# Kernel tuning notes

Measured on AMD Instinct MI355X. Metric: run time of the kernel, lower is better.

The kernel has to match this reference:

```python
import jax, jax.numpy as jnp
import numpy as np

B, S, D = 4, 2048, 1024
H, DH = 16, 64


def setup_inputs() -> dict:
    key = jax.random.key(0)
    ks = jax.random.split(key, 5)
    x = jax.random.normal(ks[0], (B, S, D), dtype=jnp.float32)
    # causal mask: True where attention is disallowed (j > i)
    mask = jnp.triu(jnp.ones((S, S), dtype=bool), k=1)
    mask = jnp.broadcast_to(mask, (B, S, S))
    scale = 1.0 / np.sqrt(D)
    w_q = jax.random.normal(ks[1], (D, D), dtype=jnp.float32) * scale
    w_k = jax.random.normal(ks[2], (D, D), dtype=jnp.float32) * scale
    w_v = jax.random.normal(ks[3], (D, D), dtype=jnp.float32) * scale
    w_o = jax.random.normal(ks[4], (D, D), dtype=jnp.float32) * scale
    return {"x": x, "mask": mask, "w_q": w_q, "w_k": w_k, "w_v": w_v, "w_o": w_o}


def reference(x, mask, w_q, w_k, w_v, w_o):
    # torch Linear: y = x @ W.T (bias=False)
    b, s, d = x.shape
    q = (x @ w_q.T).reshape(b, s, H, DH).transpose(0, 2, 1, 3)  # [B,H,S,DH]
    k = (x @ w_k.T).reshape(b, s, H, DH).transpose(0, 2, 1, 3)
    v = (x @ w_v.T).reshape(b, s, H, DH).transpose(0, 2, 1, 3)
    inv_sqrt_dh = jnp.asarray(1.0 / np.sqrt(DH), dtype=x.dtype)
    scores = jnp.einsum('bhqd,bhkd->bhqk', q * inv_sqrt_dh, k)  # [B,H,S,S]
    scores = jnp.where(mask[:, None, :, :], -jnp.inf, scores)
    attn = jax.nn.softmax(scores, axis=-1)  # dropout is identity in eval mode
    out = jnp.einsum('bhqk,bhkd->bhqd', attn, v)  # [B,H,S,DH]
    out = out.transpose(0, 2, 1, 3).reshape(b, s, d)
    out = out @ w_o.T
    return out, attn
```

## Files before the change

kernel.cpp:

```cpp
#include <hip/hip_runtime.h>

#define DEV __device__ __forceinline__

typedef __attribute__((ext_vector_type(8))) short short8;
typedef __attribute__((ext_vector_type(4))) float f32x4;

DEV unsigned short f2bf(float f) {
  unsigned u = __builtin_bit_cast(unsigned, f);
  u += 0x7fff + ((u >> 16) & 1);
  return (unsigned short)(u >> 16);
}

DEV void gload_lds16(const void* g, void* l) {
  __builtin_amdgcn_global_load_lds(
      (const __attribute__((address_space(1))) void*)g,
      (__attribute__((address_space(3))) void*)l, 16, 0, 0);
}

#if __has_builtin(__builtin_amdgcn_exp2f)
#define EXP2F(x) __builtin_amdgcn_exp2f(x)
#else
#define EXP2F(x) exp2f(x)
#endif

#define LOG2E 1.4426950408889634f
#define QSCALE (0.125f * LOG2E)
#define MFMA16(a, b, c) __builtin_amdgcn_mfma_f32_16x16x32_bf16((a), (b), (c), 0, 0, 0)

__global__ void cvt_f32_bf16(const float* __restrict__ in, unsigned short* __restrict__ out, int n4) {
  int i = blockIdx.x * blockDim.x + threadIdx.x;
  int stride = gridDim.x * blockDim.x;
  for (; i < n4; i += stride) {
    float4 v = ((const float4*)in)[i];
    ushort4 o;
    o.x = f2bf(v.x); o.y = f2bf(v.y); o.z = f2bf(v.z); o.w = f2bf(v.w);
    ((ushort4*)out)[i] = o;
  }
}

__global__ void cvt_w4(const float* __restrict__ w0, const float* __restrict__ w1,
                       const float* __restrict__ w2, const float* __restrict__ w3,
                       unsigned short* __restrict__ o0, unsigned short* __restrict__ o1,
                       unsigned short* __restrict__ o2, unsigned short* __restrict__ o3) {
  int i = blockIdx.x * blockDim.x + threadIdx.x;
  int sel = i >> 18, j = i & 0x3ffff;
  const float* in = sel == 0 ? w0 : sel == 1 ? w1 : sel == 2 ? w2 : w3;
  unsigned short* out = sel == 0 ? o0 : sel == 1 ? o1 : sel == 2 ? o2 : o3;
  float4 v = ((const float4*)in)[j];
  ushort4 o;
  o.x = f2bf(v.x); o.y = f2bf(v.y); o.z = f2bf(v.z); o.w = f2bf(v.w);
  ((ushort4*)out)[j] = o;
}

#define GK 1024
template <int MODE>
DEV void gemm_body(const unsigned short* A, const unsigned short* Bw, void* Cout,
                   int bx, int by) {
  __shared__ unsigned short Ash[128 * 32];
  __shared__ unsigned short Bsh[128 * 32];
  const int tid = threadIdx.x;
  const int lane = tid & 63;
  const int w = tid >> 6;
  const int wm = w >> 1, wn = w & 1;
  const int l15 = lane & 15, l4 = lane >> 4;
  const int row0 = by * 128;
  const int col0 = bx * 128;

  f32x4 acc[4][4] = {};

  for (int kt = 0; kt < GK; kt += 32) {
    __syncthreads();
#pragma unroll
    for (int c = 0; c < 2; ++c) {
      int o = c * 4096 + tid * 16;
      int ldsoff = c * 4096 + w * 1024;
      int row = o >> 6, colb = o & 63;
      gload_lds16((const char*)A + (size_t)(row0 + row) * 2048 + kt * 2 + colb,
                  (char*)Ash + ldsoff);
      gload_lds16((const char*)Bw + (size_t)(col0 + row) * 2048 + kt * 2 + colb,
                  (char*)Bsh + ldsoff);
    }
    __syncthreads();
    short8 af[4], bf[4];
#pragma unroll
    for (int m = 0; m < 4; ++m)
      af[m] = *(const short8*)((const char*)Ash + (wm * 64 + m * 16 + l15) * 64 + l4 * 16);
#pragma unroll
    for (int n = 0; n < 4; ++n)
      bf[n] = *(const short8*)((const char*)Bsh + (wn * 64 + n * 16 + l15) * 64 + l4 * 16);
#pragma unroll
    for (int m = 0; m < 4; ++m)
#pragma unroll
      for (int n = 0; n < 4; ++n)
        acc[m][n] = MFMA16(af[m], bf[n], acc[m][n]);
  }

#pragma unroll
  for (int m = 0; m < 4; ++m)
#pragma unroll
    for (int n = 0; n < 4; ++n)
#pragma unroll
      for (int r = 0; r < 4; ++r) {
        int mrow = row0 + wm * 64 + m * 16 + l4 * 4 + r;
        int ncol = col0 + wn * 64 + n * 16 + l15;
        float v = acc[m][n][r];
        if (MODE == 0) {
          ((unsigned short*)Cout)[(size_t)mrow * 1024 + ncol] = f2bf(v);
        } else if (MODE == 1) {
          int b = mrow >> 11, s = mrow & 2047, h = ncol >> 6, d = ncol & 63;
          ((unsigned short*)Cout)[((size_t)((b * 16 + h) * 64 + d)) * 2048 + s] = f2bf(v);
        } else if (MODE == 2) {
          ((float*)Cout)[(size_t)mrow * 1024 + ncol] = v;
        } else {
          ((unsigned short*)Cout)[(size_t)mrow * 1024 + ncol] = f2bf(v * QSCALE);
        }
      }
}

__global__ __launch_bounds__(256) void gemm_qkv(const unsigned short* __restrict__ A,
                                                const unsigned short* __restrict__ Wq,
                                                const unsigned short* __restrict__ Wk,
                                                const unsigned short* __restrict__ Wv,
                                                unsigned short* __restrict__ Qo,
                                                unsigned short* __restrict__ Ko,
                                                unsigned short* __restrict__ Vto) {
  const int z = blockIdx.z;
  if (z == 0)      gemm_body<3>(A, Wq, Qo,  blockIdx.x, blockIdx.y);
  else if (z == 1) gemm_body<0>(A, Wk, Ko,  blockIdx.x, blockIdx.y);
  else             gemm_body<1>(A, Wv, Vto, blockIdx.x, blockIdx.y);
}

__global__ __launch_bounds__(256) void gemm_out(const unsigned short* __restrict__ A,
                                                const unsigned short* __restrict__ Bw,
                                                float* __restrict__ Cout) {
  gemm_body<2>(A, Bw, Cout, blockIdx.x, blockIdx.y);
}


DEV void stage_tile(const unsigned short* src_base, size_t row_stride, int col0,
                    char* ldsbase, int tid) {
  const int w = tid >> 6;
  const int r0 = tid >> 3;
  const int c0 = (tid & 7) ^ (r0 & 7);
  gload_lds16((const char*)(src_base + (size_t)r0 * row_stride + col0 + c0 * 8),
              ldsbase + w * 1024);
  const int r1 = 32 + r0;
  gload_lds16((const char*)(src_base + (size_t)r1 * row_stride + col0 + c0 * 8),
              ldsbase + 4096 + w * 1024);
}

__global__ __launch_bounds__(256, 4) void attn_fused(const unsigned short* __restrict__ Q,
                                                     const unsigned short* __restrict__ Kb,
                                                     const unsigned short* __restrict__ Vt,
                                                     float* __restrict__ attn,
                                                     unsigned short* __restrict__ O) {
  __shared__ char lds[40960];

  const int tid = threadIdx.x, lane = tid & 63, w = tid >> 6;
  const int l15 = lane & 15, l4 = lane >> 4;
  const int s7 = l15 & 7;
  const int off0 = (l4 ^ s7) << 4;
  const int off1 = ((l4 + 4) ^ s7) << 4;
  const int F = blockIdx.x;
  const int xcd = F & 7, slot = F >> 3;
  const int g = slot >> 4, r = slot & 15;
  const int pr = ((g >> 1) & 1) ? (15 - r) : r;
  const int bh = xcd + (g << 3);
  const int b = bh >> 4, h = bh & 15;

  const int qt0 = pr, qt1 = 31 - pr;
  const int q00 = qt0 * 64 + w * 16, q01 = qt1 * 64 + w * 16;
  const int myq0 = q00 + l15, myq1 = q01 + l15;

  const size_t qk_base = ((size_t)b * 2048) * 1024 + h * 64;
  const unsigned short* Qp = Q + qk_base;
  const unsigned short* Kp = Kb + qk_base;
  const unsigned short* Vp = Vt + (size_t)bh * 64 * 2048;
  float* Ap = attn + (size_t)bh * 2048 * 2048;
  char* pbase = lds + 32768 + w * 2048;

  float inv_l0, inv_l1;
  {
    short8 qf0[2], qf1[2];
    {
      const char* qrow0 = (const char*)(Qp + (size_t)myq0 * 1024);
      qf0[0] = *(const short8*)(qrow0 + (l4 * 8) * 2);
      qf0[1] = *(const short8*)(qrow0 + (32 + l4 * 8) * 2);
      const char* qrow1 = (const char*)(Qp + (size_t)myq1 * 1024);
      qf1[0] = *(const short8*)(qrow1 + (l4 * 8) * 2);
      qf1[1] = *(const short8*)(qrow1 + (32 + l4 * 8) * 2);
    }
    float lacc0[4] = {0.f, 0.f, 0.f, 0.f};
    float lacc1[4] = {0.f, 0.f, 0.f, 0.f};
    stage_tile(Kp, 1024, 0, lds, tid);
    stage_tile(Kp + (size_t)64 * 1024, 1024, 0, lds + 8192, tid);
    __syncthreads();
    const int nst = (qt1 + 2) >> 1;
    for (int st = 0; st < nst; ++st) {
      char* kbb = lds + (st & 1) * 16384;
      const int jt0 = 2 * st;
      if (jt0 + 2 <= qt1) {
        char* nb = lds + ((st + 1) & 1) * 16384;
        stage_tile(Kp + (size_t)(jt0 + 2) * 64 * 1024, 1024, 0, nb, tid);
        if (jt0 + 3 <= qt1)
          stage_tile(Kp + (size_t)(jt0 + 3) * 64 * 1024, 1024, 0, nb + 8192, tid);
      }
#pragma unroll
      for (int u = 0; u < 2; ++u) {
        const int jt = jt0 + u;
        if (jt > qt1) break;
        const char* kb = kbb + u * 8192;
        const int jbase = jt * 64;
        const bool diag1 = (jt == qt1);
        const bool do0 = (jt <= qt0);
        const bool diag0 = (jt == qt0);
#pragma unroll
        for (int jb = 0; jb < 4; ++jb) {
          const char* krow = kb + (jb * 16 + l15) * 128;
          short8 k0 = *(const short8*)(krow + off0);
          short8 k1 = *(const short8*)(krow + off1);
          f32x4 a1 = {};
          a1 = MFMA16(k0, qf1[0], a1);
          a1 = MFMA16(k1, qf1[1], a1);
#pragma unroll
          for (int rr = 0; rr < 4; ++rr) {
            int j = jbase + jb * 16 + l4 * 4 + rr;
            float e = EXP2F(a1[rr]);
            lacc1[rr] += (diag1 && j > myq1) ? 0.f : e;
          }
          if (do0) {
            f32x4 a0 = {};
            a0 = MFMA16(k0, qf0[0], a0);
            a0 = MFMA16(k1, qf0[1], a0);
#pragma unroll
            for (int rr = 0; rr < 4; ++rr) {
              int j = jbase + jb * 16 + l4 * 4 + rr;
              float e = EXP2F(a0[rr]);
              lacc0[rr] += (diag0 && j > myq0) ? 0.f : e;
            }
          }
        }
      }
      __syncthreads();
    }
    float lsum0 = (lacc0[0] + lacc0[1]) + (lacc0[2] + lacc0[3]);
    lsum0 += __shfl_xor(lsum0, 16);
    lsum0 += __shfl_xor(lsum0, 32);
    float lsum1 = (lacc1[0] + lacc1[1]) + (lacc1[2] + lacc1[3]);
    lsum1 += __shfl_xor(lsum1, 16);
    lsum1 += __shfl_xor(lsum1, 32);
    inv_l0 = 1.f / lsum0;
    inv_l1 = 1.f / lsum1;
  }

  for (int t = 0; t < 2; ++t) {
    const int qt = t ? qt1 : qt0;
    const float inv_l = t ? inv_l1 : inv_l0;
    const int q0 = qt * 64 + w * 16;
    const int myq = q0 + l15;

    short8 qf[2];
    {
      const char* qrow = (const char*)(Qp + (size_t)myq * 1024);
      qf[0] = *(const short8*)(qrow + (l4 * 8) * 2);
      qf[1] = *(const short8*)(qrow + (32 + l4 * 8) * 2);
    }

    f32x4 oacc[4] = {};
    stage_tile(Kp, 1024, 0, lds, tid);
    stage_tile(Vp, 2048, 0, lds + 16384, tid);
    __syncthreads();
    for (int jt = 0; jt <= qt; ++jt) {
      const char* kb = lds + (jt & 1) * 8192;
      const char* vb = lds + 16384 + (jt & 1) * 8192;
      if (jt < qt) {
        stage_tile(Kp + (size_t)(jt + 1) * 64 * 1024, 1024, 0,
                   lds + ((jt + 1) & 1) * 8192, tid);
        stage_tile(Vp, 2048, (jt + 1) * 64, lds + 16384 + ((jt + 1) & 1) * 8192, tid);
      }
      const int jbase = jt * 64;
      const bool diag = (jt == qt);
      float p[16];
#pragma unroll
      for (int jb = 0; jb < 4; ++jb) {
        const char* krow = kb + (jb * 16 + l15) * 128;
        short8 k0 = *(const short8*)(krow + off0);
        short8 k1 = *(const short8*)(krow + off1);
        f32x4 a = {};
        a = MFMA16(k0, qf[0], a);
        a = MFMA16(k1, qf[1], a);
#pragma unroll
        for (int rr = 0; rr < 4; ++rr) {
          int j = jbase + jb * 16 + l4 * 4 + rr;
          float e = EXP2F(a[rr]) * inv_l;
          p[jb * 4 + rr] = (diag && j > myq) ? 0.f : e;
        }
      }
#pragma unroll
      for (int jb = 0; jb < 4; ++jb) {
        f32x4 pv = {p[jb * 4], p[jb * 4 + 1], p[jb * 4 + 2], p[jb * 4 + 3]};
        *(f32x4*)(Ap + (size_t)myq * 2048 + jbase + jb * 16 + l4 * 4) = pv;
      }
#pragma unroll
      for (int jb = 0; jb < 4; ++jb) {
        unsigned u0 = f2bf(p[jb * 4]) | ((unsigned)f2bf(p[jb * 4 + 1]) << 16);
        unsigned u1 = f2bf(p[jb * 4 + 2]) | ((unsigned)f2bf(p[jb * 4 + 3]) << 16);
        uint2 uu; uu.x = u0; uu.y = u1;
        *(uint2*)(pbase + (jb * 2 + (l4 >> 1)) * 256 + l15 * 16 + (l4 & 1) * 8) = uu;
      }
      short8 pa0 = *(const short8*)(pbase + l4 * 256 + l15 * 16);
      short8 pa1 = *(const short8*)(pbase + (4 + l4) * 256 + l15 * 16);
#pragma unroll
      for (int db = 0; db < 4; ++db) {
        const char* vrow = vb + (db * 16 + l15) * 128;
        short8 v0 = *(const short8*)(vrow + off0);
        short8 v1 = *(const short8*)(vrow + off1);
        oacc[db] = MFMA16(pa0, v0, oacc[db]);
        oacc[db] = MFMA16(pa1, v1, oacc[db]);
      }
      __syncthreads();
    }

    for (int jt = qt + 1; jt < 32; ++jt) {
      const int jbase = jt * 64;
      f32x4 z = {};
#pragma unroll
      for (int jb = 0; jb < 4; ++jb)
        *(f32x4*)(Ap + (size_t)myq * 2048 + jbase + jb * 16 + l4 * 4) = z;
    }

#pragma unroll
    for (int db = 0; db < 4; ++db)
#pragma unroll
      for (int rr = 0; rr < 4; ++rr) {
        int q = q0 + l4 * 4 + rr;
        int d = db * 16 + l15;
        O[((size_t)b * 2048 + q) * 1024 + h * 64 + d] = f2bf(oacc[db][rr]);
      }
  }
}

extern "C" void kernel_launch(void* const* d_in, const int* in_sizes, int n_in,
                              void* d_out, int out_size, void* d_ws, size_t ws_size,
                              hipStream_t stream) {
  const float* x  = (const float*)d_in[0];
  const float* wq = (const float*)d_in[2];
  const float* wk = (const float*)d_in[3];
  const float* wv = (const float*)d_in[4];
  const float* wo = (const float*)d_in[5];

  float* out  = (float*)d_out;
  float* attn = out + (size_t)8192 * 1024;

  char* ws = (char*)d_ws;
  const size_t MB = 1 << 20;
  unsigned short* xb  = (unsigned short*)(ws);
  unsigned short* wqb = (unsigned short*)(ws + 16 * MB);
  unsigned short* wkb = (unsigned short*)(ws + 18 * MB);
  unsigned short* wvb = (unsigned short*)(ws + 20 * MB);
  unsigned short* wob = (unsigned short*)(ws + 22 * MB);
  unsigned short* Qb  = (unsigned short*)(ws + 24 * MB);
  unsigned short* Kb  = (unsigned short*)(ws + 40 * MB);
  unsigned short* Vtb = (unsigned short*)(ws + 56 * MB);
  unsigned short* Ob  = (unsigned short*)(ws + 72 * MB);

  cvt_f32_bf16<<<2048, 256, 0, stream>>>(x, xb, 8192 * 1024 / 4);
  cvt_w4<<<4096, 256, 0, stream>>>(wq, wk, wv, wo, wqb, wkb, wvb, wob);

  gemm_qkv<<<dim3(8, 64, 3), 256, 0, stream>>>(xb, wqb, wkb, wvb, Qb, Kb, Vtb);

  attn_fused<<<1024, 256, 0, stream>>>(Qb, Kb, Vtb, attn, Ob);

  gemm_out<<<dim3(8, 64), 256, 0, stream>>>(Ob, wob, out);
}
```

Measured before the change: 433.8 us.

## Load K and V fragments directly from global memory instead of LDS staging

Removes the double-buffered LDS staging of K and V tiles in both attention passes. Each wave now reads its MFMA operand fragments straight from global memory (through the caches), and LDS shrinks to the per-wave P scratch only. This eliminates block-wide __syncthreads and the async copy pipeline, and the smaller LDS footprint could raise occupancy. The cost is that all four waves read the same K/V data redundantly, the loads become latency-exposed with no prefetching, and the K rows are strided by 2 KB.

After: 689.6 us. 59.0% more time.

```diff
diff --git a/kernel.cpp b/kernel.cpp
--- a/kernel.cpp
+++ b/kernel.cpp
@@ -136,31 +136,15 @@
   gemm_body<2>(A, Bw, Cout, blockIdx.x, blockIdx.y);
 }
 
-
-DEV void stage_tile(const unsigned short* src_base, size_t row_stride, int col0,
-                    char* ldsbase, int tid) {
-  const int w = tid >> 6;
-  const int r0 = tid >> 3;
-  const int c0 = (tid & 7) ^ (r0 & 7);
-  gload_lds16((const char*)(src_base + (size_t)r0 * row_stride + col0 + c0 * 8),
-              ldsbase + w * 1024);
-  const int r1 = 32 + r0;
-  gload_lds16((const char*)(src_base + (size_t)r1 * row_stride + col0 + c0 * 8),
-              ldsbase + 4096 + w * 1024);
-}
-
 __global__ __launch_bounds__(256, 4) void attn_fused(const unsigned short* __restrict__ Q,
                                                      const unsigned short* __restrict__ Kb,
                                                      const unsigned short* __restrict__ Vt,
                                                      float* __restrict__ attn,
                                                      unsigned short* __restrict__ O) {
-  __shared__ char lds[40960];
+  __shared__ char lds[8192];
 
   const int tid = threadIdx.x, lane = tid & 63, w = tid >> 6;
   const int l15 = lane & 15, l4 = lane >> 4;
-  const int s7 = l15 & 7;
-  const int off0 = (l4 ^ s7) << 4;
-  const int off1 = ((l4 + 4) ^ s7) << 4;
   const int F = blockIdx.x;
   const int xcd = F & 7, slot = F >> 3;
   const int g = slot >> 4, r = slot & 15;
@@ -177,7 +161,7 @@
   const unsigned short* Kp = Kb + qk_base;
   const unsigned short* Vp = Vt + (size_t)bh * 64 * 2048;
   float* Ap = attn + (size_t)bh * 2048 * 2048;
-  char* pbase = lds + 32768 + w * 2048;
+  char* pbase = lds + w * 2048;
 
   float inv_l0, inv_l1;
   {
@@ -192,56 +176,37 @@
     }
     float lacc0[4] = {0.f, 0.f, 0.f, 0.f};
     float lacc1[4] = {0.f, 0.f, 0.f, 0.f};
-    stage_tile(Kp, 1024, 0, lds, tid);
-    stage_tile(Kp + (size_t)64 * 1024, 1024, 0, lds + 8192, tid);
-    __syncthreads();
-    const int nst = (qt1 + 2) >> 1;
-    for (int st = 0; st < nst; ++st) {
-      char* kbb = lds + (st & 1) * 16384;
-      const int jt0 = 2 * st;
-      if (jt0 + 2 <= qt1) {
-        char* nb = lds + ((st + 1) & 1) * 16384;
-        stage_tile(Kp + (size_t)(jt0 + 2) * 64 * 1024, 1024, 0, nb, tid);
-        if (jt0 + 3 <= qt1)
-          stage_tile(Kp + (size_t)(jt0 + 3) * 64 * 1024, 1024, 0, nb + 8192, tid);
-      }
-#pragma unroll
-      for (int u = 0; u < 2; ++u) {
-        const int jt = jt0 + u;
-        if (jt > qt1) break;
-        const char* kb = kbb + u * 8192;
-        const int jbase = jt * 64;
-        const bool diag1 = (jt == qt1);
-        const bool do0 = (jt <= qt0);
-        const bool diag0 = (jt == qt0);
-#pragma unroll
-        for (int jb = 0; jb < 4; ++jb) {
-          const char* krow = kb + (jb * 16 + l15) * 128;
-          short8 k0 = *(const short8*)(krow + off0);
-          short8 k1 = *(const short8*)(krow + off1);
-          f32x4 a1 = {};
-          a1 = MFMA16(k0, qf1[0], a1);
-          a1 = MFMA16(k1, qf1[1], a1);
+    for (int jt = 0; jt <= qt1; ++jt) {
+      const int jbase = jt * 64;
+      const bool diag1 = (jt == qt1);
+      const bool do0 = (jt <= qt0);
+      const bool diag0 = (jt == qt0);
+#pragma unroll
+      for (int jb = 0; jb < 4; ++jb) {
+        const char* krow = (const char*)(Kp + (size_t)(jbase + jb * 16 + l15) * 1024);
+        short8 k0 = *(const short8*)(krow + (l4 * 8) * 2);
+        short8 k1 = *(const short8*)(krow + (32 + l4 * 8) * 2);
+        f32x4 a1 = {};
+        a1 = MFMA16(k0, qf1[0], a1);
+        a1 = MFMA16(k1, qf1[1], a1);
+#pragma unroll
+        for (int rr = 0; rr < 4; ++rr) {
+          int j = jbase + jb * 16 + l4 * 4 + rr;
+          float e = EXP2F(a1[rr]);
+          lacc1[rr] += (diag1 && j > myq1) ? 0.f : e;
+        }
+        if (do0) {
+          f32x4 a0 = {};
+          a0 = MFMA16(k0, qf0[0], a0);
+          a0 = MFMA16(k1, qf0[1], a0);
 #pragma unroll
           for (int rr = 0; rr < 4; ++rr) {
             int j = jbase + jb * 16 + l4 * 4 + rr;
-            float e = EXP2F(a1[rr]);
-            lacc1[rr] += (diag1 && j > myq1) ? 0.f : e;
-          }
-          if (do0) {
-            f32x4 a0 = {};
-            a0 = MFMA16(k0, qf0[0], a0);
-            a0 = MFMA16(k1, qf0[1], a0);
-#pragma unroll
-            for (int rr = 0; rr < 4; ++rr) {
-              int j = jbase + jb * 16 + l4 * 4 + rr;
-              float e = EXP2F(a0[rr]);
-              lacc0[rr] += (diag0 && j > myq0) ? 0.f : e;
-            }
+            float e = EXP2F(a0[rr]);
+            lacc0[rr] += (diag0 && j > myq0) ? 0.f : e;
           }
         }
       }
-      __syncthreads();
     }
     float lsum0 = (lacc0[0] + lacc0[1]) + (lacc0[2] + lacc0[3]);
     lsum0 += __shfl_xor(lsum0, 16);
@@ -267,25 +232,22 @@
     }
 
     f32x4 oacc[4] = {};
-    stage_tile(Kp, 1024, 0, lds, tid);
-    stage_tile(Vp, 2048, 0, lds + 16384, tid);
-    __syncthreads();
     for (int jt = 0; jt <= qt; ++jt) {
-      const char* kb = lds + (jt & 1) * 8192;
-      const char* vb = lds + 16384 + (jt & 1) * 8192;
-      if (jt < qt) {
-        stage_tile(Kp + (size_t)(jt + 1) * 64 * 1024, 1024, 0,
-                   lds + ((jt + 1) & 1) * 8192, tid);
-        stage_tile(Vp, 2048, (jt + 1) * 64, lds + 16384 + ((jt + 1) & 1) * 8192, tid);
-      }
       const int jbase = jt * 64;
       const bool diag = (jt == qt);
+      short8 vf[8];
+#pragma unroll
+      for (int db = 0; db < 4; ++db) {
+        const char* vrow = (const char*)(Vp + (size_t)(db * 16 + l15) * 2048);
+        vf[db * 2]     = *(const short8*)(vrow + (jbase + l4 * 8) * 2);
+        vf[db * 2 + 1] = *(const short8*)(vrow + (jbase + 32 + l4 * 8) * 2);
+      }
       float p[16];
 #pragma unroll
       for (int jb = 0; jb < 4; ++jb) {
-        const char* krow = kb + (jb * 16 + l15) * 128;
-        short8 k0 = *(const short8*)(krow + off0);
-        short8 k1 = *(const short8*)(krow + off1);
+        const char* krow = (const char*)(Kp + (size_t)(jbase + jb * 16 + l15) * 1024);
+        short8 k0 = *(const short8*)(krow + (l4 * 8) * 2);
+        short8 k1 = *(const short8*)(krow + (32 + l4 * 8) * 2);
         f32x4 a = {};
         a = MFMA16(k0, qf[0], a);
         a = MFMA16(k1, qf[1], a);
@@ -312,13 +274,9 @@
       short8 pa1 = *(const short8*)(pbase + (4 + l4) * 256 + l15 * 16);
 #pragma unroll
       for (int db = 0; db < 4; ++db) {
-        const char* vrow = vb + (db * 16 + l15) * 128;
-        short8 v0 = *(const short8*)(vrow + off0);
-        short8 v1 = *(const short8*)(vrow + off1);
-        oacc[db] = MFMA16(pa0, v0, oacc[db]);
-        oacc[db] = MFMA16(pa1, v1, oacc[db]);
-      }
-      __syncthreads();
+        oacc[db] = MFMA16(pa0, vf[db * 2], oacc[db]);
+        oacc[db] = MFMA16(pa1, vf[db * 2 + 1], oacc[db]);
+      }
     }
 
     for (int jt = qt + 1; jt < 32; ++jt) {
```
